# Performance work log

Measured on AMD Instinct MI355X. Metric: run time of the kernel, lower is better.

Reference implementation:

```python
import jax, jax.numpy as jnp
import numpy as np

N, C, H, W = 8, 64, 128, 128
KS = 3


def setup_inputs() -> dict:
    key = jax.random.key(0)
    k1, k2, k3, k4 = jax.random.split(key, 4)
    gr = jax.random.normal(k1, (N, C, H, W), dtype=jnp.float32)
    gt = jax.random.normal(k2, (N, C, H, W), dtype=jnp.float32)
    # Conv2d(in_channel, 9*in_channel, 3, stride=1, pad=1): weight [O, I, kh, kw], bias [O]
    fan_in = C * KS * KS
    bound = 1.0 / np.sqrt(fan_in)
    Wc = jax.random.uniform(k3, (KS * KS * C, C, KS, KS), dtype=jnp.float32, minval=-bound, maxval=bound)
    bc = jax.random.uniform(k4, (KS * KS * C,), dtype=jnp.float32, minval=-bound, maxval=bound)
    return {"gr": gr, "gt": gt, "Wc": Wc, "bc": bc}


def reference(gr, gt, Wc, bc):
    # dynamic_filter = Conv2d(C, 9C, 3, 1, 1)(gt)
    filt = jax.lax.conv_general_dilated(
        gt, Wc, window_strides=(1, 1), padding=((1, 1), (1, 1)),
        dimension_numbers=("NCHW", "OIHW", "NCHW"),
    ) + bc[None, :, None, None]  # [N, 9C, H, W]

    n, c, h, w = gr.shape
    pad = (KS - 1) // 2
    # replicate padding (torch F.pad mode='replicate' == jnp 'edge')
    grp = jnp.pad(gr, ((0, 0), (0, 0), (pad, pad), (pad, pad)), mode="edge")
    # 3x3 patches as 9 shifted views: [N, C, 9, H, W], index order (kh, kw)
    patches = jnp.stack(
        [grp[:, :, i:i + h, j:j + w] for i in range(KS) for j in range(KS)], axis=2
    )
    # torch code's conv output channel layout is (c, kh, kw); its double transpose
    # of both patches and kernels cancels, so pairing is kernel[c, kh, kw] * patch[c, kh, kw]
    k = filt.reshape(n, c, KS * KS, h, w)
    return jnp.sum(patches * k, axis=2)  # [N, C, H, W]
```

## Files before the change

kernel.cpp:

```cpp
#include <hip/hip_runtime.h>
#include <stdint.h>


typedef short bf16x8 __attribute__((ext_vector_type(8)));
typedef float f32x4 __attribute__((ext_vector_type(4)));

#define ROWBLK_B 16640
#define BTAP_B   18432
#define ZERO_OFF 663552
#define GTB_OFF  (ZERO_OFF + ROWBLK_B)

__device__ __forceinline__ uint32_t f2bf(float f) {
  uint32_t x = __float_as_uint(f);
  return (x + 0x7FFFu + ((x >> 16) & 1u)) >> 16;
}

__device__ __forceinline__ void gload_lds16(const void* g, void* l) {
  __builtin_amdgcn_global_load_lds(
      (const __attribute__((address_space(1))) void*)g,
      (__attribute__((address_space(3))) void*)l, 16, 0, 0);
}

__global__ void prep_wc(const float* __restrict__ Wc, uint8_t* __restrict__ ws) {
  int ch = blockIdx.x * 256 + threadIdx.x;
  int tb = ch / 1152;
  int cw = ch - tb * 1152;
  int tap = tb >> 2, octile = tb & 3;
  int row = cw >> 3, sl = cw & 7;
  int slot = sl ^ (row & 7);
  int ic0 = slot * 8;
  int oc = octile * 144 + (row & 15) * 9 + (row >> 4);
  uint32_t p[4];
#pragma unroll
  for (int e = 0; e < 4; ++e) {
    uint32_t lo = f2bf(Wc[(oc * 64 + ic0 + 2 * e) * 9 + tap]);
    uint32_t hi = f2bf(Wc[(oc * 64 + ic0 + 2 * e + 1) * 9 + tap]);
    p[e] = lo | (hi << 16);
  }
  uint4 u; u.x = p[0]; u.y = p[1]; u.z = p[2]; u.w = p[3];
  *(uint4*)(ws + (size_t)tb * BTAP_B + (size_t)cw * 16) = u;
}

__global__ void prep_gt(const float* __restrict__ gt, uint8_t* __restrict__ ws) {
  int b = blockIdx.x;
  if (b == 1024) {
    uint4 z; z.x = z.y = z.z = z.w = 0;
    for (int i = threadIdx.x; i < 1040; i += 256)
      *(uint4*)(ws + ZERO_OFF + (size_t)i * 16) = z;
    return;
  }
  int n = b >> 7, y = b & 127;
  uint8_t* base = ws + GTB_OFF + (size_t)b * ROWBLK_B;
  for (int i = threadIdx.x; i < 1040; i += 256) {
    int r = i >> 3, sl = i & 7;
    int slot = sl ^ (r & 7);
    uint4 u; u.x = u.y = u.z = u.w = 0;
    if (r >= 1 && r <= 128) {
      int w = r - 1, ic0 = slot * 8;
      uint32_t p[4];
#pragma unroll
      for (int e = 0; e < 4; ++e) {
        uint32_t lo = f2bf(gt[((n * 64 + ic0 + 2 * e) * 128 + y) * 128 + w]);
        uint32_t hi = f2bf(gt[((n * 64 + ic0 + 2 * e + 1) * 128 + y) * 128 + w]);
        p[e] = lo | (hi << 16);
      }
      u.x = p[0]; u.y = p[1]; u.z = p[2]; u.w = p[3];
    }
    *(uint4*)(base + (size_t)i * 16) = u;
  }
}

__global__ __launch_bounds__(512, 2) void dfn_mfma(
    const float* __restrict__ gr, const float* __restrict__ bc,
    const uint8_t* __restrict__ ws, float* __restrict__ out) {
  __shared__ uint8_t smem[156928];
  uint8_t* Abuf = smem;
  uint8_t* Bbuf = smem + 83200;
  const int tid = threadIdx.x;
  const int lane = tid & 63;
  const int wv = tid >> 6;
  const int l15 = lane & 15;
  const int l4 = lane >> 4;
  const int bid = blockIdx.x;
  const int octile = (bid >> 3) & 3;
  const int nh = (bid & 7) | ((bid >> 5) << 3);
  const int n = nh >> 5;
  const int h0 = (nh & 31) * 4;

  int bo[2], aoff[3][2];
#pragma unroll
  for (int kk = 0; kk < 2; ++kk) {
    bo[kk] = l15 * 128 + ((kk * 64 + l4 * 16) ^ ((l15 & 7) << 4));
#pragma unroll
    for (int dwp = 0; dwp < 3; ++dwp) {
      int rl = l15 + dwp;
      aoff[dwp][kk] = rl * 128 + ((kk * 64 + l4 * 16) ^ ((rl & 7) << 4));
    }
  }
  int mrow[4], mcol[4];
#pragma unroll
  for (int mf = 0; mf < 4; ++mf) {
    mrow[mf] = (wv * 4 + mf) >> 3;
    mcol[mf] = ((wv * 4 + mf) & 7) * 2048;
  }

  const uint8_t* gtb = ws + GTB_OFF;
  const uint8_t* zblk = ws + ZERO_OFF;

#define ISSUE_B(T, BUFI) do {                                                 \
    const uint8_t* bsrc_ = ws + (size_t)((T) * 4 + octile) * BTAP_B;          \
    uint8_t* bdst_ = Bbuf + (BUFI) * BTAP_B;                                  \
    _Pragma("unroll")                                                         \
    for (int it = 0; it < 3; ++it) {                                          \
      int idx = it * 512 + tid;                                               \
      if (idx < 1152)                                                         \
        gload_lds16(bsrc_ + (size_t)idx * 16,                                 \
                    bdst_ + (size_t)(it * 512 + (tid & ~63)) * 16);           \
    }                                                                         \
  } while (0)

#define ISSUE_AROW(Y, SLOT) do {                                              \
    int y_ = (Y);                                                             \
    const uint8_t* src_ = (y_ >= 0 && y_ < 128)                               \
        ? (gtb + (size_t)(n * 128 + y_) * ROWBLK_B) : zblk;                   \
    uint8_t* dst_ = Abuf + (SLOT) * ROWBLK_B;                                 \
    _Pragma("unroll")                                                         \
    for (int it = 0; it < 3; ++it) {                                          \
      int idx = it * 512 + tid;                                               \
      if (idx < 1040)                                                         \
        gload_lds16(src_ + (size_t)idx * 16,                                  \
                    dst_ + (size_t)(it * 512 + (tid & ~63)) * 16);            \
    }                                                                         \
  } while (0)

#define TAP(DH, DWP, BUFI) do {                                               \
    const uint8_t* Bcur_ = Bbuf + (BUFI) * BTAP_B;                            \
    _Pragma("unroll")                                                         \
    for (int kk = 0; kk < 2; ++kk) {                                          \
      bf16x8 afr[4];                                                          \
      _Pragma("unroll")                                                       \
      for (int mf = 0; mf < 4; ++mf) {                                        \
        int idx_ = mrow[mf] + ((DH) + 1);                           \
        int slot_ = (idx_ == 5) ? 0 : idx_;     \
        afr[mf] = *(const bf16x8*)(Abuf + slot_ * ROWBLK_B + mcol[mf]         \
                                   + aoff[DWP][kk]);                          \
      }                                                                       \
      const uint8_t* baddr_ = Bcur_ + bo[kk];                                 \
      bf16x8 bq[4];                                                           \
      _Pragma("unroll")                                                       \
      for (int p = 0; p < 4; ++p)                                             \
        bq[p] = *(const bf16x8*)(baddr_ + p * 2048);                          \
      __builtin_amdgcn_s_setprio(1);                                          \
      _Pragma("unroll")                                                       \
      for (int nf = 0; nf < 9; ++nf) {                                        \
        bf16x8 bcur_ = bq[nf & 3];                                            \
        if (nf + 4 < 9)                                                       \
          bq[nf & 3] = *(const bf16x8*)(baddr_ + (nf + 4) * 2048);            \
        _Pragma("unroll")                                                     \
        for (int mf = 0; mf < 4; ++mf)                                        \
          acc[mf][nf] = __builtin_amdgcn_mfma_f32_16x16x32_bf16(              \
              bcur_, afr[mf], acc[mf][nf], 0, 0, 0);                          \
      }                                                                       \
      __builtin_amdgcn_s_setprio(0);                                          \
    }                                                                         \
  } while (0)

#pragma unroll
  for (int row = 0; row < 5; ++row) ISSUE_AROW(h0 - 1 + row, row);
  ISSUE_B(0, 0);
  ISSUE_B(1, 1);

  f32x4 acc[4][9];
#pragma unroll
  for (int nf = 0; nf < 9; ++nf) {
#pragma unroll
    for (int q = 0; q < 4; ++q) {
      float bias = bc[octile * 144 + (l4 * 4 + q) * 9 + nf];
      acc[0][nf][q] = bias; acc[1][nf][q] = bias;
      acc[2][nf][q] = bias; acc[3][nf][q] = bias;
    }
  }
  __syncthreads();

  ISSUE_B(2, 2); ISSUE_B(3, 3);
  TAP(-1, 0, 0); TAP(-1, 1, 1);
  __syncthreads();
  ISSUE_B(4, 0); ISSUE_B(5, 1);
  TAP(-1, 2, 2); TAP(0, 0, 3);
  __syncthreads();
  ISSUE_B(6, 2); ISSUE_B(7, 3);
  ISSUE_AROW(h0 + 4, 0);
  TAP(0, 1, 0); TAP(0, 2, 1);
  __syncthreads();
  ISSUE_B(8, 0);
  TAP(1, 0, 2); TAP(1, 1, 3);
  __syncthreads();
  TAP(1, 2, 0);

  const float* grb = gr + (size_t)(n * 64 + octile * 16 + l4 * 4) * 16384;
  float* outb = out + (size_t)(n * 64 + octile * 16 + l4 * 4) * 16384;
#pragma unroll
  for (int mf = 0; mf < 4; ++mf) {
    int p = (wv * 4 + mf) * 16 + l15;
    int hrow = p >> 7, w = p & 127;
    int h = h0 + hrow;
    int off[3][3];
#pragma unroll
    for (int i = 0; i < 3; ++i) {
      int yy = h + i - 1; yy = yy < 0 ? 0 : (yy > 127 ? 127 : yy);
#pragma unroll
      for (int j = 0; j < 3; ++j) {
        int xx = w + j - 1; xx = xx < 0 ? 0 : (xx > 127 ? 127 : xx);
        off[i][j] = yy * 128 + xx;
      }
    }
#pragma unroll
    for (int q = 0; q < 4; ++q) {
      const float* grc = grb + (size_t)q * 16384;
      float s = 0.f;
#pragma unroll
      for (int i = 0; i < 3; ++i)
#pragma unroll
        for (int j = 0; j < 3; ++j)
          s = fmaf(acc[mf][i * 3 + j][q], grc[off[i][j]], s);
      outb[(size_t)q * 16384 + h * 128 + w] = s;
    }
  }
}

extern "C" void kernel_launch(void* const* d_in, const int* in_sizes, int n_in,
                              void* d_out, int out_size, void* d_ws, size_t ws_size,
                              hipStream_t stream) {
  const float* gr = (const float*)d_in[0];
  const float* gt = (const float*)d_in[1];
  const float* Wc = (const float*)d_in[2];
  const float* bc = (const float*)d_in[3];
  uint8_t* ws = (uint8_t*)d_ws;
  float* out = (float*)d_out;

  prep_wc<<<162, 256, 0, stream>>>(Wc, ws);
  prep_gt<<<1025, 256, 0, stream>>>(gt, ws);
  dfn_mfma<<<1024, 512, 0, stream>>>(gr, bc, ws, out);
}
```

Baseline: 96.54 us.

## Halve block to 4 waves, each wave computing a full output row

Changes dfn_mfma from 8 waves of 512 threads to 4 waves of 256 threads. Each wave now owns one output row (8 M-fragments), so its A-fragment loads come from a single row slot and B fragments are reused across twice as many MFMAs. Cooperative global-to-LDS loads are reshaped to 5 iterations of 256 threads. The trade is twice the accumulator registers per wave (288 floats) with launch bounds of 256,1, which risks lower occupancy or spills, and fewer waves to hide LDS and memory latency.

```diff
diff --git a/kernel.cpp b/kernel.cpp
--- a/kernel.cpp
+++ b/kernel.cpp
@@ -70,7 +70,7 @@
   }
 }
 
-__global__ __launch_bounds__(512, 2) void dfn_mfma(
+__global__ __launch_bounds__(256, 1) void dfn_mfma(
     const float* __restrict__ gr, const float* __restrict__ bc,
     const uint8_t* __restrict__ ws, float* __restrict__ out) {
   __shared__ uint8_t smem[156928];
@@ -97,12 +97,6 @@
       aoff[dwp][kk] = rl * 128 + ((kk * 64 + l4 * 16) ^ ((rl & 7) << 4));
     }
   }
-  int mrow[4], mcol[4];
-#pragma unroll
-  for (int mf = 0; mf < 4; ++mf) {
-    mrow[mf] = (wv * 4 + mf) >> 3;
-    mcol[mf] = ((wv * 4 + mf) & 7) * 2048;
-  }
 
   const uint8_t* gtb = ws + GTB_OFF;
   const uint8_t* zblk = ws + ZERO_OFF;
@@ -111,11 +105,11 @@
     const uint8_t* bsrc_ = ws + (size_t)((T) * 4 + octile) * BTAP_B;          \
     uint8_t* bdst_ = Bbuf + (BUFI) * BTAP_B;                                  \
     _Pragma("unroll")                                                         \
-    for (int it = 0; it < 3; ++it) {                                          \
-      int idx = it * 512 + tid;                                               \
+    for (int it = 0; it < 5; ++it) {                                          \
+      int idx = it * 256 + tid;                                               \
       if (idx < 1152)                                                         \
         gload_lds16(bsrc_ + (size_t)idx * 16,                                 \
-                    bdst_ + (size_t)(it * 512 + (tid & ~63)) * 16);           \
+                    bdst_ + (size_t)(it * 256 + (tid & ~63)) * 16);           \
     }                                                                         \
   } while (0)
 
@@ -125,26 +119,26 @@
         ? (gtb + (size_t)(n * 128 + y_) * ROWBLK_B) : zblk;                   \
     uint8_t* dst_ = Abuf + (SLOT) * ROWBLK_B;                                 \
     _Pragma("unroll")                                                         \
-    for (int it = 0; it < 3; ++it) {                                          \
-      int idx = it * 512 + tid;                                               \
+    for (int it = 0; it < 5; ++it) {                                          \
+      int idx = it * 256 + tid;                                               \
       if (idx < 1040)                                                         \
         gload_lds16(src_ + (size_t)idx * 16,                                  \
-                    dst_ + (size_t)(it * 512 + (tid & ~63)) * 16);            \
+                    dst_ + (size_t)(it * 256 + (tid & ~63)) * 16);            \
     }                                                                         \
   } while (0)
 
+  f32x4 acc[8][9];
+
 #define TAP(DH, DWP, BUFI) do {                                               \
+    const int idxs_ = wv + (DH) + 1;                                          \
+    const uint8_t* Arow_ = Abuf + (idxs_ == 5 ? 0 : idxs_) * ROWBLK_B;        \
     const uint8_t* Bcur_ = Bbuf + (BUFI) * BTAP_B;                            \
     _Pragma("unroll")                                                         \
     for (int kk = 0; kk < 2; ++kk) {                                          \
-      bf16x8 afr[4];                                                          \
+      bf16x8 afr[8];                                                          \
       _Pragma("unroll")                                                       \
-      for (int mf = 0; mf < 4; ++mf) {                                        \
-        int idx_ = mrow[mf] + ((DH) + 1);                           \
-        int slot_ = (idx_ == 5) ? 0 : idx_;     \
-        afr[mf] = *(const bf16x8*)(Abuf + slot_ * ROWBLK_B + mcol[mf]         \
-                                   + aoff[DWP][kk]);                          \
-      }                                                                       \
+      for (int mf = 0; mf < 8; ++mf)                                          \
+        afr[mf] = *(const bf16x8*)(Arow_ + mf * 2048 + aoff[DWP][kk]);        \
       const uint8_t* baddr_ = Bcur_ + bo[kk];                                 \
       bf16x8 bq[4];                                                           \
       _Pragma("unroll")                                                       \
@@ -157,7 +151,7 @@
         if (nf + 4 < 9)                                                       \
           bq[nf & 3] = *(const bf16x8*)(baddr_ + (nf + 4) * 2048);            \
         _Pragma("unroll")                                                     \
-        for (int mf = 0; mf < 4; ++mf)                                        \
+        for (int mf = 0; mf < 8; ++mf)                                        \
           acc[mf][nf] = __builtin_amdgcn_mfma_f32_16x16x32_bf16(              \
               bcur_, afr[mf], acc[mf][nf], 0, 0, 0);                          \
       }                                                                       \
@@ -170,14 +164,13 @@
   ISSUE_B(0, 0);
   ISSUE_B(1, 1);
 
-  f32x4 acc[4][9];
 #pragma unroll
   for (int nf = 0; nf < 9; ++nf) {
 #pragma unroll
     for (int q = 0; q < 4; ++q) {
       float bias = bc[octile * 144 + (l4 * 4 + q) * 9 + nf];
-      acc[0][nf][q] = bias; acc[1][nf][q] = bias;
-      acc[2][nf][q] = bias; acc[3][nf][q] = bias;
+#pragma unroll
+      for (int mf = 0; mf < 8; ++mf) acc[mf][nf][q] = bias;
     }
   }
   __syncthreads();
@@ -199,21 +192,23 @@
 
   const float* grb = gr + (size_t)(n * 64 + octile * 16 + l4 * 4) * 16384;
   float* outb = out + (size_t)(n * 64 + octile * 16 + l4 * 4) * 16384;
-#pragma unroll
-  for (int mf = 0; mf < 4; ++mf) {
-    int p = (wv * 4 + mf) * 16 + l15;
-    int hrow = p >> 7, w = p & 127;
-    int h = h0 + hrow;
+  const int h = h0 + wv;
+  int yy_[3];
+#pragma unroll
+  for (int i = 0; i < 3; ++i) {
+    int yy = h + i - 1; yy_[i] = (yy < 0 ? 0 : (yy > 127 ? 127 : yy)) * 128;
+  }
+#pragma unroll
+  for (int mf = 0; mf < 8; ++mf) {
+    int w = mf * 16 + l15;
     int off[3][3];
 #pragma unroll
-    for (int i = 0; i < 3; ++i) {
-      int yy = h + i - 1; yy = yy < 0 ? 0 : (yy > 127 ? 127 : yy);
+    for (int i = 0; i < 3; ++i)
 #pragma unroll
       for (int j = 0; j < 3; ++j) {
         int xx = w + j - 1; xx = xx < 0 ? 0 : (xx > 127 ? 127 : xx);
-        off[i][j] = yy * 128 + xx;
+        off[i][j] = yy_[i] + xx;
       }
-    }
 #pragma unroll
     for (int q = 0; q < 4; ++q) {
       const float* grc = grb + (size_t)q * 16384;
@@ -240,5 +235,5 @@
 
   prep_wc<<<162, 256, 0, stream>>>(Wc, ws);
   prep_gt<<<1025, 256, 0, stream>>>(gt, ws);
-  dfn_mfma<<<1024, 512, 0, stream>>>(gr, bc, ws, out);
-}
+  dfn_mfma<<<1024, 256, 0, stream>>>(gr, bc, ws, out);
+}
```

Result: slower. 189.3 us (+96.1%).
